# Optimization experiments

Hardware: AMD Instinct MI355X
Metric: run time of the kernel (lower is better)

The kernel has to match this reference:

```python
import jax, jax.numpy as jnp
import numpy as np

NUM_CLASS = 3
SCORE_THRESH = 0.1
NMS_THRESH = 0.25
PRE = 512    # NMS_PRE_MAXSIZE (reduced from 4096 for memory; same algorithm)
POST = 100   # NMS_POST_MAXSIZE
EPS = 1e-8


def _cross(a, b):
    return a[..., 0] * b[..., 1] - a[..., 1] * b[..., 0]


def _corners(box):
    # box: (7,) = (x, y, z, dx, dy, dz, heading) -> BEV corners (4,2), CCW
    x, y, dx, dy, r = box[0], box[1], box[3], box[4], box[6]
    c, s = jnp.cos(r), jnp.sin(r)
    lx = jnp.array([0.5, -0.5, -0.5, 0.5]) * dx
    ly = jnp.array([0.5, 0.5, -0.5, -0.5]) * dy
    return jnp.stack([x + lx * c - ly * s, y + lx * s + ly * c], axis=-1)


def _in_box(pts, box):
    # pts (P,2): point-in-rotated-rect test in the box frame
    px, py = pts[:, 0] - box[0], pts[:, 1] - box[1]
    c, s = jnp.cos(box[6]), jnp.sin(box[6])
    u = px * c + py * s
    v = -px * s + py * c
    return (jnp.abs(u) <= box[3] * 0.5 + 1e-5) & (jnp.abs(v) <= box[4] * 0.5 + 1e-5)


def _bev_inter_area(ba, bb):
    # Exact rotated-rect intersection area (same construction as the CUDA
    # iou3d kernel: inside corners + edge intersections, angle-sorted shoelace).
    ca, cb = _corners(ba), _corners(bb)
    pa, ra = ca, jnp.roll(ca, -1, 0) - ca       # edges of a
    pb, rb = cb, jnp.roll(cb, -1, 0) - cb       # edges of b
    d = _cross(ra[:, None, :], rb[None, :, :])  # (4,4)
    dsafe = jnp.where(jnp.abs(d) > EPS, d, 1.0)
    qp = pb[None, :, :] - pa[:, None, :]
    t = _cross(qp, rb[None, :, :]) / dsafe
    u = _cross(qp, ra[:, None, :]) / dsafe
    vi = (jnp.abs(d) > EPS) & (t >= 0.0) & (t <= 1.0) & (u >= 0.0) & (u <= 1.0)
    ip = pa[:, None, :] + t[..., None] * ra[:, None, :]  # (4,4,2)
    pts = jnp.concatenate([ca, cb, ip.reshape(16, 2)], 0)          # (24,2)
    val = jnp.concatenate([_in_box(ca, bb), _in_box(cb, ba), vi.reshape(16)], 0)
    cnt = val.sum()
    ctr = (pts * val[:, None]).sum(0) / jnp.maximum(cnt, 1)
    ang = jnp.where(val, jnp.arctan2(pts[:, 1] - ctr[1], pts[:, 0] - ctr[0]), 1e9)
    o = jnp.argsort(ang)
    ps, vs = pts[o], val[o]
    ps = jnp.where(vs[:, None], ps, ps[0])  # collapse invalid onto first valid pt
    area = 0.5 * jnp.abs(_cross(ps, jnp.roll(ps, -1, 0)).sum())
    return jnp.where(cnt >= 3, area, 0.0)


def _iou3d(ba, bb):
    inter = _bev_inter_area(ba, bb)
    zt = jnp.minimum(ba[2] + ba[5] * 0.5, bb[2] + bb[5] * 0.5)
    zb = jnp.maximum(ba[2] - ba[5] * 0.5, bb[2] - bb[5] * 0.5)
    i3 = inter * jnp.maximum(zt - zb, 0.0)
    va = ba[3] * ba[4] * ba[5]
    vb = bb[3] * bb[4] * bb[5]
    return i3 / jnp.maximum(va + vb - i3, EPS)


_iou_mat = jax.vmap(jax.vmap(_iou3d, (None, 0)), (0, None))


def _nms(scores, boxes):
    # scores (K,) sorted descending; greedy suppression in score order
    valid = scores >= SCORE_THRESH
    iou = _iou_mat(boxes, boxes)  # (K,K)

    def body(sup, inp):
        row, v, i = inp
        keep = v & jnp.logical_not(sup[i])
        sup = sup | (keep & (row > NMS_THRESH))
        return sup, keep

    K = scores.shape[0]
    _, keep = jax.lax.scan(body, jnp.zeros((K,), bool), (iou, valid, jnp.arange(K)))
    return keep


def _post_one(cls_logits, boxes):
    # multi_classes_nms path: cls_preds_normalized=False -> sigmoid
    scores = jax.nn.sigmoid(cls_logits)  # (N, NUM_CLASS)
    out_b, out_s, out_l = [], [], []
    for k in range(NUM_CLASS):
        s = jnp.where(scores[:, k] >= SCORE_THRESH, scores[:, k], -1.0)
        top_s, idx = jax.lax.top_k(s, PRE)
        b = boxes[idx]
        keep = _nms(top_s, b)
        ks = jnp.where(keep, top_s, -1.0)
        os_, oi = jax.lax.top_k(ks, POST)
        ov = os_ >= SCORE_THRESH
        out_b.append(jnp.where(ov[:, None], b[oi], 0.0))
        out_s.append(jnp.where(ov, os_, 0.0))
        out_l.append((k + 1) * ov.astype(jnp.int32))  # final_labels = k + 1
    return (jnp.concatenate(out_b, 0), jnp.concatenate(out_s, 0),
            jnp.concatenate(out_l, 0))


def setup_inputs() -> dict:
    key = jax.random.key(0)
    k1, k2 = jax.random.split(key)
    B, N = 2, 100000
    batch_cls_preds = jax.random.normal(k1, (B, N, NUM_CLASS), dtype=jnp.float32)
    u = jax.random.uniform(k2, (B, N, 7), dtype=jnp.float32)
    x = u[..., 0] * 70.0
    y = u[..., 1] * 80.0 - 40.0
    z = u[..., 2] * 2.0 - 1.0
    dx = u[..., 3] * 3.0 + 1.5
    dy = u[..., 4] * 1.5 + 1.2
    dz = u[..., 5] * 1.0 + 1.3
    r = u[..., 6] * 2.0 * np.pi - np.pi
    batch_box_preds = jnp.stack([x, y, z, dx, dy, dz, r], axis=-1)
    return {"batch_cls_preds": batch_cls_preds, "batch_box_preds": batch_box_preds}


def reference(batch_cls_preds, batch_box_preds):
    # returns per-batch padded (pred_boxes (B, 3*POST, 7), pred_scores, pred_labels);
    # invalid slots are zeroed (label 0 == no detection)
    return jax.vmap(_post_one)(batch_cls_preds, batch_box_preds)
```

## Files before the change

kernel.cpp:

```cpp
#include <hip/hip_runtime.h>
#include <cstdint>

#define NCLS 3
#define NPTS 100000
#define NB 2
#define PRE 512
#define POST 100
#define SCORE_TH 0.1f
#define NMS_TH 0.25
#define CAP 1024
#define BPP 98
#define NBINS 384
#define BIN_SH 17
#define BIN_OFFW (0xBD000000u >> BIN_SH)
#define FMARG 2e-5f
#define NPROB (NB * NCLS)
#define WAVES_PER_PROB 2304
#define HPB (NCLS * NBINS)


__device__ __forceinline__ uint32_t score_key(float x)
{
    double sd = 1.0 / (1.0 + exp(-(double)x));
    float s = (float)sd;
    if (!(s >= SCORE_TH)) s = -1.0f;
    uint32_t u = __float_as_uint(s);
    return (u & 0x80000000u) ? ~u : (u | 0x80000000u);
}

__device__ __forceinline__ float fast_sig(float x)
{
    return 1.0f / (1.0f + __expf(-x));
}

__device__ __forceinline__ int fast_bin(float s)
{
    float v = (s >= SCORE_TH) ? s : -1.0f;
    uint32_t u = __float_as_uint(v);
    uint32_t kk = (u & 0x80000000u) ? ~u : (u | 0x80000000u);
    int b = (int)(kk >> BIN_SH) - (int)BIN_OFFW;
    return b < 0 ? 0 : (b > NBINS - 1 ? NBINS - 1 : b);
}

__global__ __launch_bounds__(1024) void hist_kernel(
    const float* __restrict__ cls, float* __restrict__ sf,
    uint32_t* __restrict__ hist_part)
{
    __shared__ uint32_t lh[HPB];
    for (int t = threadIdx.x; t < HPB; t += 1024) lh[t] = 0;
    __syncthreads();
    const int b = blockIdx.x / BPP, cb = blockIdx.x % BPP;
    const int i = cb * 1024 + threadIdx.x;
    if (i < NPTS) {
        const float* cp = cls + ((size_t)b * NPTS + i) * NCLS;
        #pragma unroll
        for (int k = 0; k < NCLS; ++k) {
            float sfv = fast_sig(cp[k]);
            sf[(size_t)(b * NCLS + k) * NPTS + i] = sfv;
            atomicAdd(&lh[k * NBINS + fast_bin(sfv)], 1u);
        }
    }
    __syncthreads();
    uint32_t* P = hist_part + (size_t)blockIdx.x * HPB;
    for (int t = threadIdx.x; t < HPB; t += 1024) P[t] = lh[t];
}

__global__ __launch_bounds__(512) void pivot_kernel(
    const uint32_t* __restrict__ hist_part, uint32_t* __restrict__ pivots,
    uint32_t* __restrict__ cand_cnt)
{
    const int p = blockIdx.x;
    const int b = p / NCLS, k = p % NCLS;
    const int tid = threadIdx.x;
    __shared__ uint32_t bins[NBINS];
    __shared__ uint32_t csum[128];
    if (tid < NBINS) {
        uint32_t s = 0;
        const uint32_t* base = hist_part + (size_t)b * BPP * HPB + k * NBINS + tid;
        for (int cb = 0; cb < BPP; ++cb)
            s += base[(size_t)cb * HPB];
        bins[tid] = s;
    }
    __syncthreads();
    if (tid < 128)
        csum[tid] = bins[tid * 3] + bins[tid * 3 + 1] + bins[tid * 3 + 2];
    __syncthreads();
    if (tid == 0) {
        int cum = 0, cchunk = 0;
        for (int c = 127; c >= 0; --c) {
            if (cum + (int)csum[c] >= PRE) { cchunk = c; break; }
            cum += (int)csum[c];
        }
        uint32_t pb = 0;
        for (int bin = cchunk * 3 + 2; bin >= cchunk * 3; --bin) {
            int h = (int)bins[bin];
            if (cum + h >= PRE) { pb = (uint32_t)bin; break; }
            cum += h;
        }
        pivots[p] = pb;
        cand_cnt[p] = 0;
    }
}

__global__ __launch_bounds__(1024) void compact_kernel(
    const float* __restrict__ cls, const float* __restrict__ sf,
    const uint32_t* __restrict__ pivots, uint32_t* __restrict__ cand_cnt,
    unsigned long long* __restrict__ cand)
{
    __shared__ unsigned long long stage[1024];
    __shared__ uint32_t lcnt, lbase;
    if (threadIdx.x == 0) lcnt = 0;
    __syncthreads();

    const int p = blockIdx.x / BPP, cb = blockIdx.x % BPP;
    const int i = cb * 1024 + threadIdx.x;
    const uint32_t pb = pivots[p];

    bool sv = false;
    unsigned long long entry = 0;
    if (i < NPTS) {
        float sfv = sf[(size_t)p * NPTS + i];
        if ((uint32_t)fast_bin(sfv + FMARG) >= pb) {
            const int b = p / NCLS, k = p % NCLS;
            uint32_t kk = score_key(cls[((size_t)b * NPTS + i) * NCLS + k]);
            entry = ((unsigned long long)kk << 32) | (uint32_t)(~(uint32_t)i);
            sv = true;
        }
    }
    if (sv) {
        uint32_t slot = atomicAdd(&lcnt, 1u);
        stage[slot] = entry;
    }
    __syncthreads();
    if (threadIdx.x == 0 && lcnt)
        lbase = atomicAdd(&cand_cnt[p], lcnt);
    __syncthreads();
    const uint32_t n = lcnt;
    if (n) {
        const uint32_t base = lbase;
        for (uint32_t e = threadIdx.x; e < n; e += 1024) {
            uint32_t g = base + e;
            if (g < CAP) cand[(size_t)p * CAP + g] = stage[e];
        }
    }
}

__global__ __launch_bounds__(1024) void select_kernel(
    const float* __restrict__ boxes, const unsigned long long* __restrict__ cand,
    const uint32_t* __restrict__ cand_cnt, uint32_t* __restrict__ cand_idx,
    float* __restrict__ cand_score, double* __restrict__ boxdata,
    float* __restrict__ screen)
{
    const int p = blockIdx.x;
    const int b = p / NCLS;
    const int tid = threadIdx.x;
    __shared__ unsigned long long skey[CAP];
    const int cnt = min((int)cand_cnt[p], CAP);
    skey[tid] = (tid < cnt) ? cand[(size_t)p * CAP + tid] : 0ull;
    __syncthreads();

    for (int k2 = 2; k2 <= CAP; k2 <<= 1)
        for (int j = k2 >> 1; j > 0; j >>= 1) {
            int ixj = tid ^ j;
            if (ixj > tid) {
                unsigned long long a = skey[tid], c = skey[ixj];
                bool up = ((tid & k2) == 0);
                if (up ? (a < c) : (a > c)) { skey[tid] = c; skey[ixj] = a; }
            }
            __syncthreads();
        }

    if (tid >= PRE) return;
    unsigned long long key = skey[tid];
    double* D = boxdata + (size_t)(p * PRE + tid) * 20;
    float* S = screen + (size_t)(p * PRE + tid) * 8;
    if (key == 0ull) {
        cand_idx[p * PRE + tid] = 0;
        cand_score[p * PRE + tid] = -1.0f;
        #pragma unroll
        for (int m = 0; m < 20; ++m) D[m] = 0.0;
        #pragma unroll
        for (int m = 0; m < 8; ++m) S[m] = 0.0f;
        return;
    }
    uint32_t idx = ~((uint32_t)key);
    uint32_t ov = (uint32_t)(key >> 32);
    uint32_t ub = (ov & 0x80000000u) ? (ov ^ 0x80000000u) : ~ov;
    float sc = __uint_as_float(ub);
    cand_idx[p * PRE + tid] = idx;
    cand_score[p * PRE + tid] = sc;

    const float* bp = boxes + ((size_t)b * NPTS + idx) * 7;
    double x = bp[0], y = bp[1], z = bp[2];
    double dx = bp[3], dy = bp[4], dz = bp[5], r = bp[6];
    double c = cos(r), s = sin(r);
    double hx = 0.5 * dx, hy = 0.5 * dy;
    double zlo = z - 0.5 * dz, zhi = z + 0.5 * dz;
    double rad = sqrt(hx * hx + hy * hy);
    D[0] = x; D[1] = y; D[2] = c; D[3] = s; D[4] = hx; D[5] = hy;
    D[6] = zlo; D[7] = zhi; D[8] = dx * dy * dz; D[9] = rad;
    const double lxs[4] = { hx, -hx, -hx,  hx };
    const double lys[4] = { hy,  hy, -hy, -hy };
    #pragma unroll
    for (int m = 0; m < 4; ++m) {
        D[10 + m] = x + lxs[m] * c - lys[m] * s;
        D[14 + m] = y + lxs[m] * s + lys[m] * c;
    }
    S[0] = (float)x; S[1] = (float)y; S[2] = (float)zlo; S[3] = (float)zhi;
    S[4] = (float)rad; S[5] = 0.0f; S[6] = 0.0f; S[7] = 0.0f;
}

__global__ __launch_bounds__(256) void iou_fused_kernel(
    const float* __restrict__ screen, const double* __restrict__ boxdata,
    unsigned long long* __restrict__ mask)
{
    const int W = blockIdx.x * 4 + (threadIdx.x >> 6);
    const int lane = threadIdx.x & 63;
    const int prob = W / WAVES_PER_PROB;
    int t = W - prob * WAVES_PER_PROB;
    int cell = t >> 6, r = t & 63;
    int wi = 0;
    while (cell >= 8 - wi) { cell -= 8 - wi; ++wi; }
    const int wj = wi + cell;
    const int bi = wi * 64 + r;
    const int j = wj * 64 + lane;

    bool surv = false;
    {
        const float* SA = screen + (size_t)(prob * PRE + bi) * 8;
        const float* SB = screen + (size_t)(prob * PRE + j) * 8;
        if (j > bi) {
            float4 a4 = *(const float4*)SA;
            float4 b4 = *(const float4*)SB;
            float hz = fminf(a4.w, b4.w) - fmaxf(a4.z, b4.z);
            if (hz > 0.0f) {
                float ddx = a4.x - b4.x, ddy = a4.y - b4.y;
                float rs = SA[4] + SB[4] + 0.01f;
                surv = (ddx * ddx + ddy * ddy <= rs * rs);
            }
        }
    }
    unsigned long long sm = __ballot(surv);
    unsigned long long supw = 0ull;
    const double* A = boxdata + (size_t)(prob * PRE + bi) * 20;

    while (sm) {
        int jb = __ffsll(sm) - 1;
        sm &= sm - 1ull;
        const int bj = wj * 64 + jb;
        const double* B = boxdata + (size_t)(prob * PRE + bj) * 20;

        double PX = 0.0, PY = 0.0;
        bool valid = false;
        if (lane < 8) {
            const double* S = (lane < 4) ? A : B;
            const double* O = (lane < 4) ? B : A;
            int m = lane & 3;
            PX = S[10 + m]; PY = S[14 + m];
            double rx = PX - O[0], ry = PY - O[1];
            double u =  rx * O[2] + ry * O[3];
            double v = -rx * O[3] + ry * O[2];
            valid = (fabs(u) <= O[4] + 1e-5) && (fabs(v) <= O[5] + 1e-5);
        } else if (lane < 24) {
            int e = lane - 8, m = e >> 2, nn = e & 3;
            double ax = A[10 + m], ay = A[14 + m];
            double rax = A[10 + ((m + 1) & 3)] - ax;
            double ray = A[14 + ((m + 1) & 3)] - ay;
            double bx = B[10 + nn], by = B[14 + nn];
            double rbx = B[10 + ((nn + 1) & 3)] - bx;
            double rby = B[14 + ((nn + 1) & 3)] - by;
            double d = rax * rby - ray * rbx;
            if (fabs(d) > 1e-8) {
                double qx = bx - ax, qy = by - ay;
                double tt = (qx * rby - qy * rbx) / d;
                double uu = (qx * ray - qy * rax) / d;
                valid = (tt >= 0.0 && tt <= 1.0 && uu >= 0.0 && uu <= 1.0);
                PX = ax + tt * rax; PY = ay + tt * ray;
            }
        }
        if (!valid) { PX = 0.0; PY = 0.0; }

        unsigned long long bal = __ballot(valid);
        int cnt = __popcll(bal);
        double sx = PX, sy = PY;
        #pragma unroll
        for (int off = 16; off; off >>= 1) {
            sx += __shfl_xor(sx, off);
            sy += __shfl_xor(sy, off);
        }
        int cdiv = cnt > 0 ? cnt : 1;
        double cxc = sx / cdiv, cyc = sy / cdiv;

        double ang = valid ? atan2(PY - cyc, PX - cxc) : 1e9;
        int sidx = lane;

        #pragma unroll
        for (int k = 2; k <= 32; k <<= 1) {
            #pragma unroll
            for (int jj = k >> 1; jj > 0; jj >>= 1) {
                double oang = __shfl_xor(ang, jj);
                double opx  = __shfl_xor(PX, jj);
                double opy  = __shfl_xor(PY, jj);
                int    oidx = __shfl_xor(sidx, jj);
                bool iLow = (lane & jj) == 0;
                bool dirUp = (lane & k) == 0;
                bool mineFirst = (ang < oang) || (ang == oang && sidx < oidx);
                bool keepMine = (mineFirst == (iLow == dirUp));
                if (!keepMine) { ang = oang; PX = opx; PY = opy; sidx = oidx; }
            }
        }

        double nxp = __shfl(PX, (lane + 1) & 31);
        double nyp = __shfl(PY, (lane + 1) & 31);
        double fx  = __shfl(PX, 0);
        double fy  = __shfl(PY, 0);
        bool last = (lane == cnt - 1);
        double qx = last ? fx : nxp, qy = last ? fy : nyp;
        double contrib = 0.0;
        if (lane < cnt)
            contrib = (PX - cxc) * (qy - cyc) - (PY - cyc) * (qx - cxc);
        #pragma unroll
        for (int off = 16; off; off >>= 1) contrib += __shfl_xor(contrib, off);
        double inter = (cnt >= 3) ? 0.5 * fabs(contrib) : 0.0;

        if (lane == 0) {
            double zt = fmin(A[7], B[7]);
            double zb = fmax(A[6], B[6]);
            double hz = zt - zb;
            bool sup = false;
            if (hz > 0.0) {
                double i3 = inter * hz;
                double den = A[8] + B[8] - i3;
                if (den < 1e-8) den = 1e-8;
                sup = (i3 / den) > (double)NMS_TH;
            }
            if (sup) supw |= 1ull << jb;
        }
    }

    if (lane == 0)
        mask[(size_t)(prob * PRE + bi) * 8 + wj] = supw;
}

__global__ __launch_bounds__(256) void nms_out_kernel(
    const float* __restrict__ boxes, const uint32_t* __restrict__ cand_idx,
    const float* __restrict__ cand_score,
    const unsigned long long* __restrict__ mask, float* __restrict__ out)
{
    const int p = blockIdx.x;
    const int b = p / NCLS, k = p % NCLS;
    const int tid = threadIdx.x;

    __shared__ unsigned long long smask[PRE * 8];
    __shared__ float sscore[PRE];
    __shared__ int slist[POST];
    __shared__ int scnt;

    for (int w = tid; w < PRE * 8; w += 256)
        smask[w] = mask[(size_t)p * PRE * 8 + w];
    for (int i = tid; i < PRE; i += 256)
        sscore[i] = cand_score[p * PRE + i];
    __syncthreads();

    if (tid < 64) {
        const int lane = tid;
        uint32_t supbits = 0;
        int c = 0;
        for (int i = 0; i < PRE; ++i) {
            uint32_t sb = (uint32_t)__shfl((int)supbits, i & 63);
            bool sup_i = (sb >> (i >> 6)) & 1u;
            float sc = sscore[i];
            bool keep = (sc >= SCORE_TH) && !sup_i;
            if (keep) {
                if (lane == 0) slist[c] = i;
                ++c;
                if (c >= POST) break;
                #pragma unroll
                for (int w = 0; w < 8; ++w) {
                    unsigned long long m = smask[i * 8 + w];
                    supbits |= (uint32_t)((m >> lane) & 1ull) << w;
                }
            }
        }
        if (lane == 0) scnt = c;
    }
    __syncthreads();

    const int cnt = scnt;
    for (int t = tid; t < POST; t += 256) {
        int row = b * (NCLS * POST) + k * POST + t;
        float* ob = out + (size_t)row * 7;
        float* os = out + (size_t)NB * NCLS * POST * 7 + row;
        float* ol = out + (size_t)NB * NCLS * POST * 7 + (size_t)NB * NCLS * POST + row;
        if (t < cnt) {
            int r = slist[t];
            uint32_t idx = cand_idx[p * PRE + r];
            const float* bp = boxes + ((size_t)b * NPTS + idx) * 7;
            #pragma unroll
            for (int c7 = 0; c7 < 7; ++c7) ob[c7] = bp[c7];
            *os = sscore[r];
            *ol = (float)(k + 1);
        } else {
            #pragma unroll
            for (int c7 = 0; c7 < 7; ++c7) ob[c7] = 0.0f;
            *os = 0.0f;
            *ol = 0.0f;
        }
    }
}

extern "C" void kernel_launch(void* const* d_in, const int* in_sizes, int n_in,
                              void* d_out, int out_size, void* d_ws, size_t ws_size,
                              hipStream_t stream)
{
    (void)in_sizes; (void)n_in; (void)out_size; (void)ws_size;
    const float* cls   = (const float*)d_in[0];
    const float* boxes = (const float*)d_in[1];
    float* out = (float*)d_out;

    char* ws = (char*)d_ws;
    uint32_t* pivots      = (uint32_t*)(ws);
    uint32_t* cand_cnt    = (uint32_t*)(ws + 64);
    unsigned long long* mask = (unsigned long long*)(ws + 128);
    unsigned long long* cand = (unsigned long long*)(ws + 196736);
    uint32_t* cand_idx    = (uint32_t*)(ws + 245888);
    float*    cand_score  = (float*)   (ws + 258176);
    double*   boxdata     = (double*)  (ws + 270464);
    float*    screen      = (float*)   (ws + 761984);
    float*    sf          = (float*)   (ws + 860288);
    uint32_t* hist_part   = (uint32_t*)(ws + 3260288);


    hipLaunchKernelGGL(hist_kernel, dim3(NB * BPP), dim3(1024), 0, stream,
                       cls, sf, hist_part);
    hipLaunchKernelGGL(pivot_kernel, dim3(NPROB), dim3(512), 0, stream,
                       hist_part, pivots, cand_cnt);
    hipLaunchKernelGGL(compact_kernel, dim3(NPROB * BPP), dim3(1024), 0, stream,
                       cls, sf, pivots, cand_cnt, cand);
    hipLaunchKernelGGL(select_kernel, dim3(NPROB), dim3(1024), 0, stream,
                       boxes, cand, cand_cnt, cand_idx, cand_score, boxdata, screen);
    hipLaunchKernelGGL(iou_fused_kernel, dim3(NPROB * WAVES_PER_PROB / 4),
                       dim3(256), 0, stream, screen, boxdata, mask);
    hipLaunchKernelGGL(nms_out_kernel, dim3(NPROB), dim3(256), 0, stream,
                       boxes, cand_idx, cand_score, mask, out);
}
```

Before: 142.9 us.

## Fuse histogram, pivot, compaction and sort into one per-problem kernel

Replaces four kernels (histogram, pivot, compaction, select/sort) with a single kernel that runs one 1024-thread block per (batch, class) problem. Each block builds its score histogram in shared memory, finds the pivot with a suffix scan, compacts candidates into shared memory and sorts them with a bitonic sort that uses wave shuffles for small strides. This removes three launches and the global round trips through sf, hist_part and cand. In exchange only six blocks run, and each makes two strided passes over 100k points, so parallelism in the scan phase drops sharply.

```diff
diff --git a/kernel.cpp b/kernel.cpp
--- a/kernel.cpp
+++ b/kernel.cpp
@@ -9,14 +9,12 @@
 #define SCORE_TH 0.1f
 #define NMS_TH 0.25
 #define CAP 1024
-#define BPP 98
 #define NBINS 384
 #define BIN_SH 17
 #define BIN_OFFW (0xBD000000u >> BIN_SH)
 #define FMARG 2e-5f
 #define NPROB (NB * NCLS)
 #define WAVES_PER_PROB 2304
-#define HPB (NCLS * NBINS)
 
 
 __device__ __forceinline__ uint32_t score_key(float x)
@@ -42,136 +40,87 @@
     return b < 0 ? 0 : (b > NBINS - 1 ? NBINS - 1 : b);
 }
 
-__global__ __launch_bounds__(1024) void hist_kernel(
-    const float* __restrict__ cls, float* __restrict__ sf,
-    uint32_t* __restrict__ hist_part)
-{
-    __shared__ uint32_t lh[HPB];
-    for (int t = threadIdx.x; t < HPB; t += 1024) lh[t] = 0;
-    __syncthreads();
-    const int b = blockIdx.x / BPP, cb = blockIdx.x % BPP;
-    const int i = cb * 1024 + threadIdx.x;
-    if (i < NPTS) {
-        const float* cp = cls + ((size_t)b * NPTS + i) * NCLS;
-        #pragma unroll
-        for (int k = 0; k < NCLS; ++k) {
-            float sfv = fast_sig(cp[k]);
-            sf[(size_t)(b * NCLS + k) * NPTS + i] = sfv;
-            atomicAdd(&lh[k * NBINS + fast_bin(sfv)], 1u);
-        }
-    }
-    __syncthreads();
-    uint32_t* P = hist_part + (size_t)blockIdx.x * HPB;
-    for (int t = threadIdx.x; t < HPB; t += 1024) P[t] = lh[t];
-}
-
-__global__ __launch_bounds__(512) void pivot_kernel(
-    const uint32_t* __restrict__ hist_part, uint32_t* __restrict__ pivots,
-    uint32_t* __restrict__ cand_cnt)
+__global__ __launch_bounds__(1024) void stage1_kernel(
+    const float* __restrict__ cls, const float* __restrict__ boxes,
+    uint32_t* __restrict__ cand_idx, float* __restrict__ cand_score,
+    double* __restrict__ boxdata, float* __restrict__ screen)
 {
     const int p = blockIdx.x;
     const int b = p / NCLS, k = p % NCLS;
     const int tid = threadIdx.x;
-    __shared__ uint32_t bins[NBINS];
-    __shared__ uint32_t csum[128];
-    if (tid < NBINS) {
-        uint32_t s = 0;
-        const uint32_t* base = hist_part + (size_t)b * BPP * HPB + k * NBINS + tid;
-        for (int cb = 0; cb < BPP; ++cb)
-            s += base[(size_t)cb * HPB];
-        bins[tid] = s;
-    }
-    __syncthreads();
-    if (tid < 128)
-        csum[tid] = bins[tid * 3] + bins[tid * 3 + 1] + bins[tid * 3 + 2];
-    __syncthreads();
-    if (tid == 0) {
-        int cum = 0, cchunk = 0;
-        for (int c = 127; c >= 0; --c) {
-            if (cum + (int)csum[c] >= PRE) { cchunk = c; break; }
-            cum += (int)csum[c];
-        }
-        uint32_t pb = 0;
-        for (int bin = cchunk * 3 + 2; bin >= cchunk * 3; --bin) {
-            int h = (int)bins[bin];
-            if (cum + h >= PRE) { pb = (uint32_t)bin; break; }
-            cum += h;
-        }
-        pivots[p] = pb;
-        cand_cnt[p] = 0;
-    }
-}
-
-__global__ __launch_bounds__(1024) void compact_kernel(
-    const float* __restrict__ cls, const float* __restrict__ sf,
-    const uint32_t* __restrict__ pivots, uint32_t* __restrict__ cand_cnt,
-    unsigned long long* __restrict__ cand)
-{
-    __shared__ unsigned long long stage[1024];
-    __shared__ uint32_t lcnt, lbase;
-    if (threadIdx.x == 0) lcnt = 0;
-    __syncthreads();
-
-    const int p = blockIdx.x / BPP, cb = blockIdx.x % BPP;
-    const int i = cb * 1024 + threadIdx.x;
-    const uint32_t pb = pivots[p];
-
-    bool sv = false;
-    unsigned long long entry = 0;
-    if (i < NPTS) {
-        float sfv = sf[(size_t)p * NPTS + i];
+
+    __shared__ uint32_t hist[2][NBINS];
+    __shared__ uint32_t suf[NBINS];
+    __shared__ unsigned long long skey[CAP];
+    __shared__ uint32_t lcnt;
+    __shared__ uint32_t pivot_s;
+
+    if (tid < NBINS) { hist[0][tid] = 0; hist[1][tid] = 0; }
+    if (tid == 0) { lcnt = 0; pivot_s = 0; }
+    __syncthreads();
+
+    const float* cp = cls + (size_t)b * NPTS * NCLS + k;
+    const int par = (tid >> 6) & 1;
+
+    for (int i = tid; i < NPTS; i += 1024) {
+        float x = cp[(size_t)i * NCLS];
+        atomicAdd(&hist[par][fast_bin(fast_sig(x))], 1u);
+    }
+    __syncthreads();
+
+    if (tid < NBINS) suf[tid] = hist[0][tid] + hist[1][tid];
+    __syncthreads();
+    for (int off = 1; off < NBINS; off <<= 1) {
+        uint32_t v = 0;
+        if (tid < NBINS && tid + off < NBINS) v = suf[tid + off];
+        __syncthreads();
+        if (tid < NBINS) suf[tid] += v;
+        __syncthreads();
+    }
+    if (tid < NBINS && suf[tid] >= PRE &&
+        (tid == NBINS - 1 || suf[tid + 1] < PRE))
+        pivot_s = (uint32_t)tid;
+    __syncthreads();
+    const uint32_t pb = pivot_s;
+
+    for (int i = tid; i < NPTS; i += 1024) {
+        float x = cp[(size_t)i * NCLS];
+        float sfv = fast_sig(x);
         if ((uint32_t)fast_bin(sfv + FMARG) >= pb) {
-            const int b = p / NCLS, k = p % NCLS;
-            uint32_t kk = score_key(cls[((size_t)b * NPTS + i) * NCLS + k]);
-            entry = ((unsigned long long)kk << 32) | (uint32_t)(~(uint32_t)i);
-            sv = true;
-        }
-    }
-    if (sv) {
-        uint32_t slot = atomicAdd(&lcnt, 1u);
-        stage[slot] = entry;
-    }
-    __syncthreads();
-    if (threadIdx.x == 0 && lcnt)
-        lbase = atomicAdd(&cand_cnt[p], lcnt);
-    __syncthreads();
-    const uint32_t n = lcnt;
-    if (n) {
-        const uint32_t base = lbase;
-        for (uint32_t e = threadIdx.x; e < n; e += 1024) {
-            uint32_t g = base + e;
-            if (g < CAP) cand[(size_t)p * CAP + g] = stage[e];
-        }
-    }
-}
-
-__global__ __launch_bounds__(1024) void select_kernel(
-    const float* __restrict__ boxes, const unsigned long long* __restrict__ cand,
-    const uint32_t* __restrict__ cand_cnt, uint32_t* __restrict__ cand_idx,
-    float* __restrict__ cand_score, double* __restrict__ boxdata,
-    float* __restrict__ screen)
-{
-    const int p = blockIdx.x;
-    const int b = p / NCLS;
-    const int tid = threadIdx.x;
-    __shared__ unsigned long long skey[CAP];
-    const int cnt = min((int)cand_cnt[p], CAP);
-    skey[tid] = (tid < cnt) ? cand[(size_t)p * CAP + tid] : 0ull;
-    __syncthreads();
-
-    for (int k2 = 2; k2 <= CAP; k2 <<= 1)
-        for (int j = k2 >> 1; j > 0; j >>= 1) {
-            int ixj = tid ^ j;
-            if (ixj > tid) {
-                unsigned long long a = skey[tid], c = skey[ixj];
-                bool up = ((tid & k2) == 0);
-                if (up ? (a < c) : (a > c)) { skey[tid] = c; skey[ixj] = a; }
-            }
+            uint32_t kk = score_key(x);
+            unsigned long long entry =
+                ((unsigned long long)kk << 32) | (uint32_t)(~(uint32_t)i);
+            uint32_t slot = atomicAdd(&lcnt, 1u);
+            if (slot < CAP) skey[slot] = entry;
+        }
+    }
+    __syncthreads();
+    const uint32_t cnt = lcnt < CAP ? lcnt : CAP;
+    for (uint32_t e = tid; e < CAP; e += 1024)
+        if (e >= cnt) skey[e] = 0ull;
+    __syncthreads();
+
+    unsigned long long val = skey[tid];
+    for (int k2 = 2; k2 <= CAP; k2 <<= 1) {
+        const bool up = (tid & k2) == 0;
+        for (int j = k2 >> 1; j >= 64; j >>= 1) {
+            skey[tid] = val;
             __syncthreads();
-        }
+            unsigned long long o = skey[tid ^ j];
+            __syncthreads();
+            const bool keepLarge = (((tid & j) == 0) == up);
+            val = keepLarge ? (val >= o ? val : o) : (val <= o ? val : o);
+        }
+        int js = (k2 >> 1) < 32 ? (k2 >> 1) : 32;
+        for (int j = js; j >= 1; j >>= 1) {
+            unsigned long long o = __shfl_xor(val, j);
+            const bool keepLarge = (((tid & j) == 0) == up);
+            val = keepLarge ? (val >= o ? val : o) : (val <= o ? val : o);
+        }
+    }
 
     if (tid >= PRE) return;
-    unsigned long long key = skey[tid];
+    unsigned long long key = val;
     double* D = boxdata + (size_t)(p * PRE + tid) * 20;
     float* S = screen + (size_t)(p * PRE + tid) * 8;
     if (key == 0ull) {
@@ -419,26 +368,14 @@
     float* out = (float*)d_out;
 
     char* ws = (char*)d_ws;
-    uint32_t* pivots      = (uint32_t*)(ws);
-    uint32_t* cand_cnt    = (uint32_t*)(ws + 64);
-    unsigned long long* mask = (unsigned long long*)(ws + 128);
-    unsigned long long* cand = (unsigned long long*)(ws + 196736);
-    uint32_t* cand_idx    = (uint32_t*)(ws + 245888);
-    float*    cand_score  = (float*)   (ws + 258176);
-    double*   boxdata     = (double*)  (ws + 270464);
-    float*    screen      = (float*)   (ws + 761984);
-    float*    sf          = (float*)   (ws + 860288);
-    uint32_t* hist_part   = (uint32_t*)(ws + 3260288);
-
-
-    hipLaunchKernelGGL(hist_kernel, dim3(NB * BPP), dim3(1024), 0, stream,
-                       cls, sf, hist_part);
-    hipLaunchKernelGGL(pivot_kernel, dim3(NPROB), dim3(512), 0, stream,
-                       hist_part, pivots, cand_cnt);
-    hipLaunchKernelGGL(compact_kernel, dim3(NPROB * BPP), dim3(1024), 0, stream,
-                       cls, sf, pivots, cand_cnt, cand);
-    hipLaunchKernelGGL(select_kernel, dim3(NPROB), dim3(1024), 0, stream,
-                       boxes, cand, cand_cnt, cand_idx, cand_score, boxdata, screen);
+    unsigned long long* mask = (unsigned long long*)(ws);
+    uint32_t* cand_idx    = (uint32_t*)(ws + 196608);
+    float*    cand_score  = (float*)   (ws + 208896);
+    double*   boxdata     = (double*)  (ws + 221184);
+    float*    screen      = (float*)   (ws + 712704);
+
+    hipLaunchKernelGGL(stage1_kernel, dim3(NPROB), dim3(1024), 0, stream,
+                       cls, boxes, cand_idx, cand_score, boxdata, screen);
     hipLaunchKernelGGL(iou_fused_kernel, dim3(NPROB * WAVES_PER_PROB / 4),
                        dim3(256), 0, stream, screen, boxdata, mask);
     hipLaunchKernelGGL(nms_out_kernel, dim3(NPROB), dim3(256), 0, stream,
```

Result: slower. 202.8 us (+41.9%).
